# Kernel optimization log

Measured on AMD Instinct MI355X. Metric: run time of the kernel, lower is better.

The kernel has to match this reference:

```python
import jax, jax.numpy as jnp
import numpy as np

B = 32; NMAX = 256; E = 512; H = 512; U = 256; M = 32; L = 2; P = 4; TAU = 1.0
S = NMAX + 1                      # pseudo-seq len = nodes + SOS
IN0 = E + (M - 1) + P             # GRU layer-0 input size


def setup_inputs() -> dict:
    key = jax.random.key(0)
    ks = jax.random.split(key, 22)
    f = lambda k, sh, sc=0.05: jax.random.normal(k, sh, dtype=jnp.float32) * sc
    return {
        "h_padded": jax.random.normal(ks[0], (B, NMAX, E), jnp.float32),
        "hg": jax.random.normal(ks[1], (B, E), jnp.float32),
        "num_nodes": jax.random.randint(ks[2], (B,), 1, NMAX + 1),
        "u_noise": jax.random.uniform(ks[3], (M, B, S), jnp.float32),
        "emb_special": f(ks[4], (2, E), 1.0),
        "emb_pos": f(ks[5], (M, P), 1.0),
        "Wp": f(ks[6], (L * H, E)), "bp": f(ks[7], (L * H,)),
        "W_ih0": f(ks[8], (3 * H, IN0)), "W_hh0": f(ks[9], (3 * H, H)),
        "b_ih0": f(ks[10], (3 * H,)), "b_hh0": f(ks[11], (3 * H,)),
        "W_ih1": f(ks[12], (3 * H, H)), "W_hh1": f(ks[13], (3 * H, H)),
        "b_ih1": f(ks[14], (3 * H,)), "b_hh1": f(ks[15], (3 * H,)),
        "W1": f(ks[16], (U, H)), "W2": f(ks[17], (U, H)),
        "wc": f(ks[18], (U,)), "V": f(ks[19], (U,)),
        "Wf": f(ks[20], (M - 1, H)), "bf": f(ks[21], (M - 1,)),
    }


def _gru_step(x, hid, params):
    # torch nn.GRU single time step, L layers; gate order (r, z, n)
    new = []
    inp = x
    for l, (Wi, Wh, bi, bh) in enumerate(params):
        hp = hid[l]
        gi = inp @ Wi.T + bi
        gh = hp @ Wh.T + bh
        gi_r, gi_z, gi_n = jnp.split(gi, 3, axis=-1)
        gh_r, gh_z, gh_n = jnp.split(gh, 3, axis=-1)
        r = jax.nn.sigmoid(gi_r + gh_r)
        z = jax.nn.sigmoid(gi_z + gh_z)
        n = jnp.tanh(gi_n + r * gh_n)
        hn = (1.0 - z) * n + z * hp
        new.append(hn)
        inp = hn
    return inp, jnp.stack(new, 0)


def reference(h_padded, hg, num_nodes, u_noise, emb_special, emb_pos, Wp, bp,
              W_ih0, W_hh0, b_ih0, b_hh0, W_ih1, W_hh1, b_ih1, b_hh1,
              W1, W2, wc, V, Wf, bf):
    lens = num_nodes + 1
    mask = jnp.arange(S)[None, :] < lens[:, None]                       # [B,S]
    node_valid = (jnp.arange(NMAX)[None, :] < num_nodes[:, None]).astype(h_padded.dtype)
    # encoder_out = [SOS emb ; h nodes ; zero pad] as pad_sequence would give
    sos_enc = jnp.broadcast_to(emb_special[1], (B, 1, E))
    encoder_out = jnp.concatenate([sos_enc, h_padded * node_valid[..., None]], axis=1)  # [B,S,E]
    enc_W1 = encoder_out @ W1.T                                          # [B,S,U] hoisted (loop-invariant)
    dec_hidden = jnp.tanh(hg @ Wp.T + bp).reshape(B, L, H).transpose(1, 0, 2)  # [L,B,H]
    theta0 = jnp.zeros((B, M - 1), encoder_out.dtype)
    dec_input = jnp.concatenate([jnp.broadcast_to(emb_special[0], (B, E)), theta0], axis=1)
    cov_vec0 = jnp.zeros((B, S), encoder_out.dtype)
    gumbel = -jnp.log(-jnp.log(u_noise + 1e-10) + 1e-10)                 # [M,B,S]
    gru_params = ((W_ih0, W_hh0, b_ih0, b_hh0), (W_ih1, W_hh1, b_ih1, b_hh1))
    neg = jnp.float32(-1e30)

    def step(carry, xs):
        dec_in, hid, cov_vec, cov_loss = carry
        i, pe, g = xs
        x = jnp.concatenate([dec_in, jnp.broadcast_to(pe, (B, P))], axis=1)
        out, hid = _gru_step(x, hid, gru_params)                        # out [B,H]
        # Bahdanau attention with coverage
        uj = enc_W1 + (out @ W2.T)[:, None, :] + cov_vec[..., None] * wc
        uj = jnp.tanh(uj) @ V                                           # [B,S]
        aj = jax.nn.softmax(jnp.where(mask, uj, neg), axis=-1)
        # hard gumbel-softmax (straight-through)
        logits = jnp.log(aj + 1e-12)
        y = jax.nn.softmax((logits + g) / TAU, axis=1)
        onehot = jax.nn.one_hot(jnp.argmax(y, axis=1), S, dtype=y.dtype)
        hard = jax.lax.stop_gradient(onehot - y) + y
        chosen = jnp.einsum('bse,bs->be', encoder_out, hard)            # [B,E]
        cov_loss = cov_loss + jnp.minimum(aj, cov_vec).sum()
        cov_vec = cov_vec + aj
        theta = jnp.where(i < 1,
                          jnp.zeros((B, M - 1), out.dtype),
                          jax.nn.sigmoid(out @ Wf.T + bf))
        dec_next = jnp.concatenate([chosen, theta], axis=1)
        return (dec_next, hid, cov_vec, cov_loss), (hard, theta, aj)

    init = (dec_input, dec_hidden, cov_vec0, jnp.float32(0.0))
    xs = (jnp.arange(M), emb_pos, gumbel)
    carry_f, (hards, thetas, ajs) = jax.lax.scan(step, init, xs)
    cov_loss = carry_f[3] / B
    pointer = jnp.transpose(hards, (1, 2, 0))   # [B,S,M]
    adj = jnp.transpose(thetas, (1, 2, 0))      # [B,M-1,M]
    atts = jnp.transpose(ajs, (1, 2, 0))        # [B,S,M]
    return pointer, cov_loss, encoder_out, adj, atts
```

## Files before the change

### kernel.cpp

```cpp
#include <hip/hip_runtime.h>

constexpr int NB  = 32;
constexpr int NMX = 256;
constexpr int ED  = 512;
constexpr int HD  = 512;
constexpr int UD  = 256;
constexpr int MS  = 32;
constexpr int PD  = 4;
constexpr int SD  = 257;
constexpr int IL0 = 547;
constexpr int NI4_0 = 137;
constexpr int NI4_1 = 128;

constexpr long long OFF_PTR  = 0;
constexpr long long OFF_COVL = (long long)NB*SD*MS;
constexpr long long OFF_ENC  = OFF_COVL + 1;
constexpr long long OFF_ADJ  = OFF_ENC + (long long)NB*SD*ED;
constexpr long long OFF_ATT  = OFF_ADJ + (long long)NB*(MS-1)*MS;

__device__ __forceinline__ float sigf(float x){ return 1.0f/(1.0f + __expf(-x)); }
__device__ __forceinline__ float ftanh(float x){ float e = __expf(2.0f*x); return 1.0f - 2.0f/(e + 1.0f); }

__global__ void k_enc(const float* __restrict__ hp, const float* __restrict__ embsp,
                      const int* __restrict__ nn, float* __restrict__ out){
  int r = blockIdx.x; int b = r / SD, s = r % SD;
  float* dst = out + OFF_ENC + (long long)r*ED;
  int t = threadIdx.x;
  if (s == 0){
    const float* src = embsp + ED;
    int e = t*4; float4 v = *(const float4*)(src + e);
    dst[e] = v.x; dst[e+1] = v.y; dst[e+2] = v.z; dst[e+3] = v.w;
  } else if (s-1 < nn[b]){
    const float* src = hp + ((long long)b*NMX + (s-1))*ED;
    int e = t*4; float4 v = *(const float4*)(src + e);
    dst[e] = v.x; dst[e+1] = v.y; dst[e+2] = v.z; dst[e+3] = v.w;
  } else {
    int e = t*4;
    dst[e] = 0.f; dst[e+1] = 0.f; dst[e+2] = 0.f; dst[e+3] = 0.f;
  }
}

__global__ void k_misc(const float* __restrict__ hg, const float* __restrict__ embsp,
                       const float* __restrict__ embpos, const float* __restrict__ W1,
                       const float* __restrict__ Wih0, const float* __restrict__ W2,
                       float* __restrict__ x4, float* __restrict__ hg4,
                       float* __restrict__ cov, float* __restrict__ covl,
                       float* __restrict__ W1T, float* __restrict__ Wih0_4,
                       float* __restrict__ W2T){
  int idx = blockIdx.x*blockDim.x + threadIdx.x;
  const int N0 = 548*NB;
  const int N1 = N0 + ED*NB;
  const int N2 = N1 + NB*SD;
  const int N3 = N2 + NB;
  const int N4 = N3 + UD*ED;
  const int N5 = N4 + 1536*548;
  const int N6 = N5 + ED*UD;
  for (int i = idx; i < N6; i += gridDim.x*blockDim.x){
    if (i < N0){
      int kb = i >> 7, r = i & 3;
      int k = kb*4 + r;
      float v;
      if (k < ED) v = embsp[k];
      else if (k < ED + MS - 1) v = 0.f;
      else if (k < IL0) v = embpos[k - (ED + MS - 1)];
      else v = 0.f;
      x4[i] = v;
    } else if (i < N1){
      int j = i - N0;
      int kb = j >> 7, b = (j >> 2) & 31, r = j & 3;
      hg4[j] = hg[(long long)b*ED + kb*4 + r];
    } else if (i < N2){
      cov[i - N1] = 0.f;
    } else if (i < N3){
      covl[i - N2] = 0.f;
    } else if (i < N4){
      int j = i - N3; int k = j / UD, u = j % UD;
      W1T[j] = W1[(long long)u*ED + k];
    } else if (i < N5){
      int j = i - N4; int row = j / 548, c = j % 548;
      Wih0_4[j] = (c < IL0) ? Wih0[(long long)row*IL0 + c] : 0.f;
    } else {
      int j = i - N5; int k = j / UD, u = j % UD;
      W2T[j] = W2[(long long)u*HD + k];
    }
  }
}

__global__ __launch_bounds__(256) void k_encw1(const float* __restrict__ out,
                        const float4* __restrict__ W1T4, float4* __restrict__ encW1){
  __shared__ __align__(16) float As[16][68];
  __shared__ __align__(16) float Bs[16][68];
  int t = threadIdx.x;
  int bm = blockIdx.x >> 2, bn = blockIdx.x & 3;
  int m0 = bm*64, n0 = bn*64;
  const float* A = out + OFF_ENC;
  int tm = t >> 4, tn = t & 15;
  float4 acc[4];
  #pragma unroll
  for (int i = 0; i < 4; ++i) acc[i] = {0.f,0.f,0.f,0.f};
  int arow = t >> 2, akq = t & 3;
  int bk = t >> 4, bnq = t & 15;
  for (int k0 = 0; k0 < 512; k0 += 16){
    float av[4];
    bool okA = (m0 + arow) < NB*SD;
    long long abase = (long long)(m0 + arow)*ED + k0 + akq*4;
    #pragma unroll
    for (int j = 0; j < 4; ++j) av[j] = okA ? A[abase + j] : 0.f;
    float4 bv = W1T4[(long long)(k0 + bk)*64 + (n0 >> 2) + bnq];
    __syncthreads();
    #pragma unroll
    for (int j = 0; j < 4; ++j) As[akq*4 + j][arow] = av[j];
    *(float4*)&Bs[bk][bnq*4] = bv;
    __syncthreads();
    #pragma unroll
    for (int kk = 0; kk < 16; ++kk){
      float4 a = *(const float4*)&As[kk][tm*4];
      float4 bq = *(const float4*)&Bs[kk][tn*4];
      acc[0].x += a.x*bq.x; acc[0].y += a.x*bq.y; acc[0].z += a.x*bq.z; acc[0].w += a.x*bq.w;
      acc[1].x += a.y*bq.x; acc[1].y += a.y*bq.y; acc[1].z += a.y*bq.z; acc[1].w += a.y*bq.w;
      acc[2].x += a.z*bq.x; acc[2].y += a.z*bq.y; acc[2].z += a.z*bq.z; acc[2].w += a.z*bq.w;
      acc[3].x += a.w*bq.x; acc[3].y += a.w*bq.y; acc[3].z += a.w*bq.z; acc[3].w += a.w*bq.w;
    }
  }
  #pragma unroll
  for (int i = 0; i < 4; ++i){
    int r = m0 + tm*4 + i;
    if (r < NB*SD) encW1[(long long)r*64 + (n0 >> 2) + tn] = acc[i];
  }
}

__global__ void k_hid0(const float4* __restrict__ hg4, const float4* __restrict__ Wp4,
                       const float* __restrict__ bp, float* __restrict__ h0,
                       float* __restrict__ h1){
  int t = threadIdx.x; int b = t & 31;
  int row = blockIdx.x*8 + (t >> 5);
  const float4* w = Wp4 + (long long)row*128;
  float acc = bp[row];
  #pragma unroll 4
  for (int i = 0; i < 128; ++i){
    float4 wv = w[i], xv = hg4[i*NB + b];
    acc += wv.x*xv.x + wv.y*xv.y + wv.z*xv.z + wv.w*xv.w;
  }
  float v = ftanh(acc);
  int h = row & 511;
  int idx = (h >> 2)*128 + b*4 + (h & 3);
  if (row < HD) h0[idx] = v;
  else          h1[idx] = v;
}

template<int NI4>
__global__ __launch_bounds__(512) void k_gru(const float4* __restrict__ x4,
                      const float4* __restrict__ h4,
                      const float4* __restrict__ Wih4, const float4* __restrict__ Whh4,
                      const float* __restrict__ bih, const float* __restrict__ bhh,
                      float* __restrict__ outT){
  __shared__ float part[2][NB][8][6];
  int t = threadIdx.x;
  int b = t & 31, ks = (t >> 5) & 7, hl = (t >> 8) & 1;
  int h = blockIdx.x*2 + hl;
  float ai0 = 0.f, ai1 = 0.f, ai2 = 0.f, ah0 = 0.f, ah1 = 0.f, ah2 = 0.f;
  {
    const float4* w0 = Wih4 + (long long)(0*HD + h)*NI4;
    const float4* w1 = Wih4 + (long long)(1*HD + h)*NI4;
    const float4* w2 = Wih4 + (long long)(2*HD + h)*NI4;
    int s0 = (ks*NI4) >> 3, e0 = ((ks + 1)*NI4) >> 3;
    for (int kb = s0; kb < e0; ++kb){
      float4 xv = x4[kb*NB + b];
      float4 a = w0[kb], c = w1[kb], d = w2[kb];
      ai0 += xv.x*a.x + xv.y*a.y + xv.z*a.z + xv.w*a.w;
      ai1 += xv.x*c.x + xv.y*c.y + xv.z*c.z + xv.w*c.w;
      ai2 += xv.x*d.x + xv.y*d.y + xv.z*d.z + xv.w*d.w;
    }
  }
  {
    const float4* w0 = Whh4 + (long long)(0*HD + h)*128;
    const float4* w1 = Whh4 + (long long)(1*HD + h)*128;
    const float4* w2 = Whh4 + (long long)(2*HD + h)*128;
    int s1 = ks*16, e1 = s1 + 16;
    for (int kb = s1; kb < e1; ++kb){
      float4 xv = h4[kb*NB + b];
      float4 a = w0[kb], c = w1[kb], d = w2[kb];
      ah0 += xv.x*a.x + xv.y*a.y + xv.z*a.z + xv.w*a.w;
      ah1 += xv.x*c.x + xv.y*c.y + xv.z*c.z + xv.w*c.w;
      ah2 += xv.x*d.x + xv.y*d.y + xv.z*d.z + xv.w*d.w;
    }
  }
  part[hl][b][ks][0] = ai0; part[hl][b][ks][1] = ai1; part[hl][b][ks][2] = ai2;
  part[hl][b][ks][3] = ah0; part[hl][b][ks][4] = ah1; part[hl][b][ks][5] = ah2;
  __syncthreads();
  if (t < 64){
    int b2 = t & 31, hl2 = t >> 5;
    int h2 = blockIdx.x*2 + hl2;
    float g0=0.f,g1=0.f,g2=0.f,g3=0.f,g4=0.f,g5=0.f;
    #pragma unroll
    for (int k = 0; k < 8; ++k){
      g0 += part[hl2][b2][k][0]; g1 += part[hl2][b2][k][1]; g2 += part[hl2][b2][k][2];
      g3 += part[hl2][b2][k][3]; g4 += part[hl2][b2][k][4]; g5 += part[hl2][b2][k][5];
    }
    float gir = g0 + bih[h2], giz = g1 + bih[HD + h2], gin = g2 + bih[2*HD + h2];
    float ghr = g3 + bhh[h2], ghz = g4 + bhh[HD + h2], ghn = g5 + bhh[2*HD + h2];
    float r = sigf(gir + ghr);
    float z = sigf(giz + ghz);
    float nn = ftanh(gin + r*ghn);
    int idx = (h2 >> 2)*128 + b2*4 + (h2 & 3);
    float hp = ((const float*)h4)[idx];
    outT[idx] = (1.f - z)*nn + z*hp;
  }
}

__global__ __launch_bounds__(512) void k_qs(const float4* __restrict__ h1,
                      const float4* __restrict__ W2T4, const float4* __restrict__ Wf4,
                      const float* __restrict__ bfv, const float* __restrict__ embpos,
                      int m, const float4* __restrict__ encW1,
                      const float4* __restrict__ wc4, const float4* __restrict__ V4,
                      const float* __restrict__ cov, float* __restrict__ sc,
                      float* __restrict__ x4, float* __restrict__ out){
  __shared__ __align__(16) float h1s[512];
  __shared__ __align__(16) float wcs[256];
  __shared__ __align__(16) float Vs[256];
  __shared__ __align__(16) float qs[256];
  __shared__ __align__(16) float4 qpart[8][64];
  int t = threadIdx.x;
  int b = blockIdx.x >> 3, seg = blockIdx.x & 7;
  if (t < 128) ((float4*)h1s)[t] = h1[t*NB + b];
  else if (t < 192) ((float4*)wcs)[t - 128] = wc4[t - 128];
  else if (t < 256) ((float4*)Vs)[t - 192] = V4[t - 192];
  __syncthreads();
  {
    int u4 = t & 63, kq = t >> 6;
    float4 acc = {0.f,0.f,0.f,0.f};
    const float4* w = W2T4 + (long long)(kq*64)*64 + u4;
    const float* hh = h1s + kq*64;
    #pragma unroll 4
    for (int k = 0; k < 64; ++k){
      float a = hh[k];
      float4 wv = w[(long long)k*64];
      acc.x += a*wv.x; acc.y += a*wv.y; acc.z += a*wv.z; acc.w += a*wv.w;
    }
    qpart[kq][u4] = acc;
  }
  __syncthreads();
  if (t < 64){
    float4 s = qpart[0][t];
    #pragma unroll
    for (int k = 1; k < 8; ++k){
      float4 p = qpart[k][t];
      s.x += p.x; s.y += p.y; s.z += p.z; s.w += p.w;
    }
    ((float4*)qs)[t] = s;
  } else if (seg == 0){
    int w = (t >> 6) - 1;
    int lane = t & 63;
    for (int j = w; j < MS-1; j += 7){
      const float4* wf = Wf4 + (long long)j*128 + lane*2;
      float4 w0 = wf[0], w1v = wf[1];
      const float4* hh4 = (const float4*)h1s + lane*2;
      float4 hv0 = hh4[0], hv1 = hh4[1];
      float d = w0.x*hv0.x + w0.y*hv0.y + w0.z*hv0.z + w0.w*hv0.w
              + w1v.x*hv1.x + w1v.y*hv1.y + w1v.z*hv1.z + w1v.w*hv1.w;
      for (int off = 32; off; off >>= 1) d += __shfl_xor(d, off);
      if (lane == 0){
        float th = (m < 1) ? 0.f : sigf(d + bfv[j]);
        out[OFF_ADJ + (long long)b*(MS-1)*MS + (long long)j*MS + m] = th;
        int k = ED + j;
        x4[(k >> 2)*128 + b*4 + (k & 3)] = th;
      }
    }
  }
  if (seg == 0 && t == 0 && m + 1 < MS){
    #pragma unroll
    for (int p = 0; p < PD; ++p){
      int k = ED + MS - 1 + p;
      x4[(k >> 2)*128 + b*4 + (k & 3)] = embpos[(m+1)*PD + p];
    }
  }
  __syncthreads();
  int lane = t & 63, wav = t >> 6;
  int s0 = seg*33;
  float4 q4 = ((const float4*)qs)[lane];
  float4 wv = ((const float4*)wcs)[lane];
  float4 vv = ((const float4*)Vs)[lane];
  for (int s = s0 + wav; s < s0 + 33 && s < SD; s += 8){
    float cv = cov[b*SD + s];
    float4 e4 = encW1[((long long)b*SD + s)*64 + lane];
    float acc = vv.x*ftanh(e4.x + q4.x + cv*wv.x)
              + vv.y*ftanh(e4.y + q4.y + cv*wv.y)
              + vv.z*ftanh(e4.z + q4.z + cv*wv.z)
              + vv.w*ftanh(e4.w + q4.w + cv*wv.w);
    for (int off = 32; off; off >>= 1) acc += __shfl_xor(acc, off);
    if (lane == 0) sc[b*SD + s] = acc;
  }
}

__global__ __launch_bounds__(512) void k_soft(const float* __restrict__ sc,
                      const int* __restrict__ nn, const float* __restrict__ un, int m,
                      float* __restrict__ cov, float* __restrict__ covl,
                      float* __restrict__ out, float4* __restrict__ x4,
                      const float* __restrict__ enc){
  __shared__ float red[8]; __shared__ float redc[8]; __shared__ int redi[8];
  __shared__ float s_mx, s_den; __shared__ int s_k;
  int b = blockIdx.x, t = threadIdx.x;
  int lane = t & 63, wav = t >> 6;
  int n = nn[b];
  float sv = (t < SD) ? sc[b*SD + t] : -3.4e38f;
  float cv = (t < SD) ? cov[b*SD + t] : 0.f;
  float v1 = (t < SD && t <= n) ? sv : -3.4e38f;
  for (int off = 32; off; off >>= 1) v1 = fmaxf(v1, __shfl_xor(v1, off));
  if (lane == 0) red[wav] = v1;
  __syncthreads();
  if (t == 0){
    float mm = red[0];
    for (int i = 1; i < 8; ++i) mm = fmaxf(mm, red[i]);
    s_mx = mm;
  }
  __syncthreads();
  float ev = (t < SD && t <= n) ? __expf(sv - s_mx) : 0.f;
  float v2 = ev;
  for (int off = 32; off; off >>= 1) v2 += __shfl_xor(v2, off);
  if (lane == 0) red[wav] = v2;
  __syncthreads();
  if (t == 0){
    float ss = 0.f;
    for (int i = 0; i < 8; ++i) ss += red[i];
    s_den = ss;
  }
  __syncthreads();
  float aj = (t < SD) ? ev / s_den : 0.f;
  float yl = -3.4e38f; int idx = SD; float lcl = 0.f;
  if (t < SD){
    float u = un[((long long)m*NB + b)*SD + t];
    float g = -__logf(-__logf(u + 1e-10f) + 1e-10f);
    yl = __logf(aj + 1e-12f) + g;
    idx = t;
    lcl = fminf(aj, cv);
    cov[b*SD + t] = cv + aj;
    out[OFF_ATT + ((long long)b*SD + t)*MS + m] = aj;
  }
  for (int off = 32; off; off >>= 1){
    float oy = __shfl_xor(yl, off); int oi = __shfl_xor(idx, off);
    if (oy > yl || (oy == yl && oi < idx)){ yl = oy; idx = oi; }
  }
  for (int off = 32; off; off >>= 1) lcl += __shfl_xor(lcl, off);
  if (lane == 0){ red[wav] = yl; redi[wav] = idx; redc[wav] = lcl; }
  __syncthreads();
  if (t == 0){
    float by = red[0]; int bi = redi[0]; float cl = redc[0];
    for (int w = 1; w < 8; ++w){
      if (red[w] > by || (red[w] == by && redi[w] < bi)){ by = red[w]; bi = redi[w]; }
      cl += redc[w];
    }
    s_k = bi;
    covl[b] += cl;
  }
  __syncthreads();
  int kk = s_k;
  if (t < SD) out[OFF_PTR + ((long long)b*SD + t)*MS + m] = (t == kk) ? 1.f : 0.f;
  const float* er = enc + ((long long)b*SD + kk)*ED;
  if (t < 128){
    float4 v; v.x = er[t*4]; v.y = er[t*4+1]; v.z = er[t*4+2]; v.w = er[t*4+3];
    x4[t*NB + b] = v;
  }
}

__global__ void k_fin(const float* __restrict__ covl, float* __restrict__ out){
  if (threadIdx.x == 0 && blockIdx.x == 0){
    float s = 0.f;
    for (int i = 0; i < NB; ++i) s += covl[i];
    out[OFF_COVL] = s / (float)NB;
  }
}

extern "C" void kernel_launch(void* const* d_in, const int* in_sizes, int n_in,
                              void* d_out, int out_size, void* d_ws, size_t ws_size,
                              hipStream_t stream){
  const float* h_padded    = (const float*)d_in[0];
  const float* hg          = (const float*)d_in[1];
  const int*   num_nodes   = (const int*)  d_in[2];
  const float* u_noise     = (const float*)d_in[3];
  const float* emb_special = (const float*)d_in[4];
  const float* emb_pos     = (const float*)d_in[5];
  const float* Wp          = (const float*)d_in[6];
  const float* bp          = (const float*)d_in[7];
  const float* W_ih0       = (const float*)d_in[8];
  const float* W_hh0       = (const float*)d_in[9];
  const float* b_ih0       = (const float*)d_in[10];
  const float* b_hh0       = (const float*)d_in[11];
  const float* W_ih1       = (const float*)d_in[12];
  const float* W_hh1       = (const float*)d_in[13];
  const float* b_ih1       = (const float*)d_in[14];
  const float* b_hh1       = (const float*)d_in[15];
  const float* W1          = (const float*)d_in[16];
  const float* W2          = (const float*)d_in[17];
  const float* wc          = (const float*)d_in[18];
  const float* V           = (const float*)d_in[19];
  const float* Wf          = (const float*)d_in[20];
  const float* bf          = (const float*)d_in[21];
  float* out = (float*)d_out;

  float* ws      = (float*)d_ws;
  float* encW1   = ws;  ws += (long long)NB*SD*UD;
  float* Wih0_4  = ws;  ws += (long long)1536*548;
  float* W1T     = ws;  ws += (long long)UD*ED;
  float* W2T     = ws;  ws += (long long)UD*ED;
  float* x4      = ws;  ws += 548*NB;
  float* hg4     = ws;  ws += ED*NB;
  float* h0      = ws;  ws += 2*HD*NB;
  float* h1      = ws;  ws += 2*HD*NB;
  float* cov     = ws;  ws += NB*SD;
  float* covl    = ws;  ws += NB;
  float* sc      = ws;  ws += NB*SD;

  k_enc  <<<NB*SD, 128, 0, stream>>>(h_padded, emb_special, num_nodes, out);
  k_misc <<<256, 256, 0, stream>>>(hg, emb_special, emb_pos, W1, W_ih0, W2,
                                   x4, hg4, cov, covl, W1T, Wih0_4, W2T);
  k_encw1<<<516, 256, 0, stream>>>(out, (const float4*)W1T, (float4*)encW1);
  k_hid0 <<<128, 256, 0, stream>>>((const float4*)hg4, (const float4*)Wp, bp, h0, h1);

  for (int m = 0; m < MS; ++m){
    float* h0c = h0 + (m & 1)*HD*NB;
    float* h0n = h0 + ((m + 1) & 1)*HD*NB;
    float* h1c = h1 + (m & 1)*HD*NB;
    float* h1n = h1 + ((m + 1) & 1)*HD*NB;
    k_gru<NI4_0><<<256, 512, 0, stream>>>((const float4*)x4, (const float4*)h0c,
        (const float4*)Wih0_4, (const float4*)W_hh0, b_ih0, b_hh0, h0n);
    k_gru<NI4_1><<<256, 512, 0, stream>>>((const float4*)h0n, (const float4*)h1c,
        (const float4*)W_ih1, (const float4*)W_hh1, b_ih1, b_hh1, h1n);
    k_qs  <<<256, 512, 0, stream>>>((const float4*)h1n, (const float4*)W2T,
        (const float4*)Wf, bf, emb_pos, m, (const float4*)encW1,
        (const float4*)wc, (const float4*)V, cov, sc, x4, out);
    k_soft<<<NB, 512, 0, stream>>>(sc, num_nodes, u_noise, m, cov, covl, out,
        (float4*)x4, out + OFF_ENC);
  }
  k_fin<<<1, 64, 0, stream>>>(covl, out);
}
```

Baseline: 1.427 ms.

## Fuse attention scoring with softmax kernel, retile encW1 GEMM, unroll GRU loops

Merges the per-step query/score kernel and the softmax/sampling kernel into one 1024-thread block per batch row, keeping scores in shared memory and dropping one launch per decoder step. The cost is that each step's attention now runs on only 32 blocks instead of 256. The layer-0 GRU input is padded to 576 so the reduction splits evenly into fixed-length, fully unrolled loops. The encW1 GEMM tile grows to 128 rows with 8 accumulators per thread, halving the grid.

```diff
diff --git a/kernel.cpp b/kernel.cpp
--- a/kernel.cpp
+++ b/kernel.cpp
@@ -9,8 +9,8 @@
 constexpr int PD  = 4;
 constexpr int SD  = 257;
 constexpr int IL0 = 547;
-constexpr int NI4_0 = 137;
-constexpr int NI4_1 = 128;
+constexpr int XP  = 576;
+constexpr int XP4 = 144;
 
 constexpr long long OFF_PTR  = 0;
 constexpr long long OFF_COVL = (long long)NB*SD*MS;
@@ -48,12 +48,12 @@
                        float* __restrict__ W1T, float* __restrict__ Wih0_4,
                        float* __restrict__ W2T){
   int idx = blockIdx.x*blockDim.x + threadIdx.x;
-  const int N0 = 548*NB;
+  const int N0 = XP*NB;
   const int N1 = N0 + ED*NB;
   const int N2 = N1 + NB*SD;
   const int N3 = N2 + NB;
   const int N4 = N3 + UD*ED;
-  const int N5 = N4 + 1536*548;
+  const int N5 = N4 + 1536*XP;
   const int N6 = N5 + ED*UD;
   for (int i = idx; i < N6; i += gridDim.x*blockDim.x){
     if (i < N0){
@@ -77,7 +77,7 @@
       int j = i - N3; int k = j / UD, u = j % UD;
       W1T[j] = W1[(long long)u*ED + k];
     } else if (i < N5){
-      int j = i - N4; int row = j / 548, c = j % 548;
+      int j = i - N4; int row = j / XP, c = j % XP;
       Wih0_4[j] = (c < IL0) ? Wih0[(long long)row*IL0 + c] : 0.f;
     } else {
       int j = i - N5; int k = j / UD, u = j % UD;
@@ -88,43 +88,48 @@
 
 __global__ __launch_bounds__(256) void k_encw1(const float* __restrict__ out,
                         const float4* __restrict__ W1T4, float4* __restrict__ encW1){
-  __shared__ __align__(16) float As[16][68];
+  __shared__ __align__(16) float As[16][132];
   __shared__ __align__(16) float Bs[16][68];
   int t = threadIdx.x;
   int bm = blockIdx.x >> 2, bn = blockIdx.x & 3;
-  int m0 = bm*64, n0 = bn*64;
+  int m0 = bm*128, n0 = bn*64;
   const float* A = out + OFF_ENC;
   int tm = t >> 4, tn = t & 15;
-  float4 acc[4];
+  float4 acc[8];
   #pragma unroll
-  for (int i = 0; i < 4; ++i) acc[i] = {0.f,0.f,0.f,0.f};
-  int arow = t >> 2, akq = t & 3;
-  int bk = t >> 4, bnq = t & 15;
+  for (int i = 0; i < 8; ++i) acc[i] = {0.f,0.f,0.f,0.f};
+  int arow = t >> 1, ac2 = t & 1;
+  int bk = t >> 4, bn4 = t & 15;
   for (int k0 = 0; k0 < 512; k0 += 16){
-    float av[4];
-    bool okA = (m0 + arow) < NB*SD;
-    long long abase = (long long)(m0 + arow)*ED + k0 + akq*4;
-    #pragma unroll
-    for (int j = 0; j < 4; ++j) av[j] = okA ? A[abase + j] : 0.f;
-    float4 bv = W1T4[(long long)(k0 + bk)*64 + (n0 >> 2) + bnq];
+    float av[8];
+    int rr = m0 + arow; if (rr >= NB*SD) rr = NB*SD - 1;
+    long long abase = (long long)rr*ED + k0 + ac2*8;
+    #pragma unroll
+    for (int j = 0; j < 8; ++j) av[j] = A[abase + j];
+    float4 bv = W1T4[(long long)(k0 + bk)*64 + (n0 >> 2) + bn4];
     __syncthreads();
     #pragma unroll
-    for (int j = 0; j < 4; ++j) As[akq*4 + j][arow] = av[j];
-    *(float4*)&Bs[bk][bnq*4] = bv;
+    for (int j = 0; j < 8; ++j) As[ac2*8 + j][arow] = av[j];
+    *(float4*)&Bs[bk][bn4*4] = bv;
     __syncthreads();
     #pragma unroll
     for (int kk = 0; kk < 16; ++kk){
-      float4 a = *(const float4*)&As[kk][tm*4];
+      float4 a0 = *(const float4*)&As[kk][tm*8];
+      float4 a1 = *(const float4*)&As[kk][tm*8 + 4];
       float4 bq = *(const float4*)&Bs[kk][tn*4];
-      acc[0].x += a.x*bq.x; acc[0].y += a.x*bq.y; acc[0].z += a.x*bq.z; acc[0].w += a.x*bq.w;
-      acc[1].x += a.y*bq.x; acc[1].y += a.y*bq.y; acc[1].z += a.y*bq.z; acc[1].w += a.y*bq.w;
-      acc[2].x += a.z*bq.x; acc[2].y += a.z*bq.y; acc[2].z += a.z*bq.z; acc[2].w += a.z*bq.w;
-      acc[3].x += a.w*bq.x; acc[3].y += a.w*bq.y; acc[3].z += a.w*bq.z; acc[3].w += a.w*bq.w;
+      acc[0].x += a0.x*bq.x; acc[0].y += a0.x*bq.y; acc[0].z += a0.x*bq.z; acc[0].w += a0.x*bq.w;
+      acc[1].x += a0.y*bq.x; acc[1].y += a0.y*bq.y; acc[1].z += a0.y*bq.z; acc[1].w += a0.y*bq.w;
+      acc[2].x += a0.z*bq.x; acc[2].y += a0.z*bq.y; acc[2].z += a0.z*bq.z; acc[2].w += a0.z*bq.w;
+      acc[3].x += a0.w*bq.x; acc[3].y += a0.w*bq.y; acc[3].z += a0.w*bq.z; acc[3].w += a0.w*bq.w;
+      acc[4].x += a1.x*bq.x; acc[4].y += a1.x*bq.y; acc[4].z += a1.x*bq.z; acc[4].w += a1.x*bq.w;
+      acc[5].x += a1.y*bq.x; acc[5].y += a1.y*bq.y; acc[5].z += a1.y*bq.z; acc[5].w += a1.y*bq.w;
+      acc[6].x += a1.z*bq.x; acc[6].y += a1.z*bq.y; acc[6].z += a1.z*bq.z; acc[6].w += a1.z*bq.w;
+      acc[7].x += a1.w*bq.x; acc[7].y += a1.w*bq.y; acc[7].z += a1.w*bq.z; acc[7].w += a1.w*bq.w;
     }
   }
   #pragma unroll
-  for (int i = 0; i < 4; ++i){
-    int r = m0 + tm*4 + i;
+  for (int i = 0; i < 8; ++i){
+    int r = m0 + tm*8 + i;
     if (r < NB*SD) encW1[(long long)r*64 + (n0 >> 2) + tn] = acc[i];
   }
 }
@@ -148,24 +153,26 @@
   else          h1[idx] = v;
 }
 
-template<int NI4>
+template<int PER>
 __global__ __launch_bounds__(512) void k_gru(const float4* __restrict__ x4,
                       const float4* __restrict__ h4,
                       const float4* __restrict__ Wih4, const float4* __restrict__ Whh4,
                       const float* __restrict__ bih, const float* __restrict__ bhh,
                       float* __restrict__ outT){
+  constexpr int NI4 = PER*8;
   __shared__ float part[2][NB][8][6];
   int t = threadIdx.x;
   int b = t & 31, ks = (t >> 5) & 7, hl = (t >> 8) & 1;
   int h = blockIdx.x*2 + hl;
   float ai0 = 0.f, ai1 = 0.f, ai2 = 0.f, ah0 = 0.f, ah1 = 0.f, ah2 = 0.f;
   {
-    const float4* w0 = Wih4 + (long long)(0*HD + h)*NI4;
-    const float4* w1 = Wih4 + (long long)(1*HD + h)*NI4;
-    const float4* w2 = Wih4 + (long long)(2*HD + h)*NI4;
-    int s0 = (ks*NI4) >> 3, e0 = ((ks + 1)*NI4) >> 3;
-    for (int kb = s0; kb < e0; ++kb){
-      float4 xv = x4[kb*NB + b];
+    const float4* w0 = Wih4 + (long long)(0*HD + h)*NI4 + ks*PER;
+    const float4* w1 = Wih4 + (long long)(1*HD + h)*NI4 + ks*PER;
+    const float4* w2 = Wih4 + (long long)(2*HD + h)*NI4 + ks*PER;
+    const float4* xb = x4 + (long long)(ks*PER)*NB + b;
+    #pragma unroll
+    for (int kb = 0; kb < PER; ++kb){
+      float4 xv = xb[kb*NB];
       float4 a = w0[kb], c = w1[kb], d = w2[kb];
       ai0 += xv.x*a.x + xv.y*a.y + xv.z*a.z + xv.w*a.w;
       ai1 += xv.x*c.x + xv.y*c.y + xv.z*c.z + xv.w*c.w;
@@ -173,12 +180,13 @@
     }
   }
   {
-    const float4* w0 = Whh4 + (long long)(0*HD + h)*128;
-    const float4* w1 = Whh4 + (long long)(1*HD + h)*128;
-    const float4* w2 = Whh4 + (long long)(2*HD + h)*128;
-    int s1 = ks*16, e1 = s1 + 16;
-    for (int kb = s1; kb < e1; ++kb){
-      float4 xv = h4[kb*NB + b];
+    const float4* w0 = Whh4 + (long long)(0*HD + h)*128 + ks*16;
+    const float4* w1 = Whh4 + (long long)(1*HD + h)*128 + ks*16;
+    const float4* w2 = Whh4 + (long long)(2*HD + h)*128 + ks*16;
+    const float4* hb = h4 + (long long)(ks*16)*NB + b;
+    #pragma unroll
+    for (int kb = 0; kb < 16; ++kb){
+      float4 xv = hb[kb*NB];
       float4 a = w0[kb], c = w1[kb], d = w2[kb];
       ah0 += xv.x*a.x + xv.y*a.y + xv.z*a.z + xv.w*a.w;
       ah1 += xv.x*c.x + xv.y*c.y + xv.z*c.z + xv.w*c.w;
@@ -208,50 +216,44 @@
   }
 }
 
-__global__ __launch_bounds__(512) void k_qs(const float4* __restrict__ h1,
+__global__ __launch_bounds__(1024) void k_attn2(const float4* __restrict__ h1,
                       const float4* __restrict__ W2T4, const float4* __restrict__ Wf4,
                       const float* __restrict__ bfv, const float* __restrict__ embpos,
                       int m, const float4* __restrict__ encW1,
                       const float4* __restrict__ wc4, const float4* __restrict__ V4,
-                      const float* __restrict__ cov, float* __restrict__ sc,
-                      float* __restrict__ x4, float* __restrict__ out){
+                      const int* __restrict__ nn, const float* __restrict__ un,
+                      float* __restrict__ cov, float* __restrict__ covl,
+                      float* __restrict__ out, float* __restrict__ x4,
+                      const float* __restrict__ enc){
   __shared__ __align__(16) float h1s[512];
   __shared__ __align__(16) float wcs[256];
   __shared__ __align__(16) float Vs[256];
   __shared__ __align__(16) float qs[256];
   __shared__ __align__(16) float4 qpart[8][64];
-  int t = threadIdx.x;
-  int b = blockIdx.x >> 3, seg = blockIdx.x & 7;
+  __shared__ float scs[SD];
+  __shared__ float red[16]; __shared__ float redc[16]; __shared__ int redi[16];
+  __shared__ float s_mx, s_den; __shared__ int s_k;
+  int t = threadIdx.x, b = blockIdx.x;
+  int lane = t & 63, wav = t >> 6;
   if (t < 128) ((float4*)h1s)[t] = h1[t*NB + b];
   else if (t < 192) ((float4*)wcs)[t - 128] = wc4[t - 128];
   else if (t < 256) ((float4*)Vs)[t - 192] = V4[t - 192];
   __syncthreads();
-  {
-    int u4 = t & 63, kq = t >> 6;
+  if (t < 512){
+    int kq = t >> 6, u4 = t & 63;
     float4 acc = {0.f,0.f,0.f,0.f};
     const float4* w = W2T4 + (long long)(kq*64)*64 + u4;
     const float* hh = h1s + kq*64;
-    #pragma unroll 4
+    #pragma unroll 8
     for (int k = 0; k < 64; ++k){
       float a = hh[k];
       float4 wv = w[(long long)k*64];
       acc.x += a*wv.x; acc.y += a*wv.y; acc.z += a*wv.z; acc.w += a*wv.w;
     }
     qpart[kq][u4] = acc;
-  }
-  __syncthreads();
-  if (t < 64){
-    float4 s = qpart[0][t];
-    #pragma unroll
-    for (int k = 1; k < 8; ++k){
-      float4 p = qpart[k][t];
-      s.x += p.x; s.y += p.y; s.z += p.z; s.w += p.w;
-    }
-    ((float4*)qs)[t] = s;
-  } else if (seg == 0){
-    int w = (t >> 6) - 1;
-    int lane = t & 63;
-    for (int j = w; j < MS-1; j += 7){
+  } else if (wav < 15){
+    int w0i = wav - 8;
+    for (int j = w0i; j < MS-1; j += 7){
       const float4* wf = Wf4 + (long long)j*128 + lane*2;
       float4 w0 = wf[0], w1v = wf[1];
       const float4* hh4 = (const float4*)h1s + lane*2;
@@ -266,8 +268,7 @@
         x4[(k >> 2)*128 + b*4 + (k & 3)] = th;
       }
     }
-  }
-  if (seg == 0 && t == 0 && m + 1 < MS){
+  } else if (t == 1023 && m + 1 < MS){
     #pragma unroll
     for (int p = 0; p < PD; ++p){
       int k = ED + MS - 1 + p;
@@ -275,59 +276,56 @@
     }
   }
   __syncthreads();
-  int lane = t & 63, wav = t >> 6;
-  int s0 = seg*33;
-  float4 q4 = ((const float4*)qs)[lane];
-  float4 wv = ((const float4*)wcs)[lane];
-  float4 vv = ((const float4*)Vs)[lane];
-  for (int s = s0 + wav; s < s0 + 33 && s < SD; s += 8){
-    float cv = cov[b*SD + s];
-    float4 e4 = encW1[((long long)b*SD + s)*64 + lane];
-    float acc = vv.x*ftanh(e4.x + q4.x + cv*wv.x)
-              + vv.y*ftanh(e4.y + q4.y + cv*wv.y)
-              + vv.z*ftanh(e4.z + q4.z + cv*wv.z)
-              + vv.w*ftanh(e4.w + q4.w + cv*wv.w);
-    for (int off = 32; off; off >>= 1) acc += __shfl_xor(acc, off);
-    if (lane == 0) sc[b*SD + s] = acc;
-  }
-}
-
-__global__ __launch_bounds__(512) void k_soft(const float* __restrict__ sc,
-                      const int* __restrict__ nn, const float* __restrict__ un, int m,
-                      float* __restrict__ cov, float* __restrict__ covl,
-                      float* __restrict__ out, float4* __restrict__ x4,
-                      const float* __restrict__ enc){
-  __shared__ float red[8]; __shared__ float redc[8]; __shared__ int redi[8];
-  __shared__ float s_mx, s_den; __shared__ int s_k;
-  int b = blockIdx.x, t = threadIdx.x;
-  int lane = t & 63, wav = t >> 6;
+  if (t < 256){
+    const float* fp = (const float*)qpart;
+    float s = 0.f;
+    #pragma unroll
+    for (int k = 0; k < 8; ++k) s += fp[k*256 + t];
+    qs[t] = s;
+  }
+  __syncthreads();
+  {
+    float4 q4 = ((const float4*)qs)[lane];
+    float4 wv = ((const float4*)wcs)[lane];
+    float4 vv = ((const float4*)Vs)[lane];
+    for (int s = wav; s < SD; s += 16){
+      float cv = cov[b*SD + s];
+      float4 e4 = encW1[((long long)b*SD + s)*64 + lane];
+      float acc = vv.x*ftanh(e4.x + q4.x + cv*wv.x)
+                + vv.y*ftanh(e4.y + q4.y + cv*wv.y)
+                + vv.z*ftanh(e4.z + q4.z + cv*wv.z)
+                + vv.w*ftanh(e4.w + q4.w + cv*wv.w);
+      for (int off = 32; off; off >>= 1) acc += __shfl_xor(acc, off);
+      if (lane == 0) scs[s] = acc;
+    }
+  }
+  __syncthreads();
   int n = nn[b];
-  float sv = (t < SD) ? sc[b*SD + t] : -3.4e38f;
-  float cv = (t < SD) ? cov[b*SD + t] : 0.f;
-  float v1 = (t < SD && t <= n) ? sv : -3.4e38f;
+  float v1 = (t < SD && t <= n) ? scs[t] : -3.4e38f;
   for (int off = 32; off; off >>= 1) v1 = fmaxf(v1, __shfl_xor(v1, off));
   if (lane == 0) red[wav] = v1;
   __syncthreads();
   if (t == 0){
     float mm = red[0];
-    for (int i = 1; i < 8; ++i) mm = fmaxf(mm, red[i]);
+    for (int i = 1; i < 16; ++i) mm = fmaxf(mm, red[i]);
     s_mx = mm;
   }
   __syncthreads();
-  float ev = (t < SD && t <= n) ? __expf(sv - s_mx) : 0.f;
+  float ev = (t < SD && t <= n) ? __expf(scs[t] - s_mx) : 0.f;
   float v2 = ev;
   for (int off = 32; off; off >>= 1) v2 += __shfl_xor(v2, off);
   if (lane == 0) red[wav] = v2;
   __syncthreads();
   if (t == 0){
     float ss = 0.f;
-    for (int i = 0; i < 8; ++i) ss += red[i];
+    for (int i = 0; i < 16; ++i) ss += red[i];
     s_den = ss;
   }
   __syncthreads();
   float aj = (t < SD) ? ev / s_den : 0.f;
   float yl = -3.4e38f; int idx = SD; float lcl = 0.f;
   if (t < SD){
+    float cv = cov[b*SD + t];
     float u = un[((long long)m*NB + b)*SD + t];
     float g = -__logf(-__logf(u + 1e-10f) + 1e-10f);
     yl = __logf(aj + 1e-12f) + g;
@@ -345,7 +343,7 @@
   __syncthreads();
   if (t == 0){
     float by = red[0]; int bi = redi[0]; float cl = redc[0];
-    for (int w = 1; w < 8; ++w){
+    for (int w = 1; w < 16; ++w){
       if (red[w] > by || (red[w] == by && redi[w] < bi)){ by = red[w]; bi = redi[w]; }
       cl += redc[w];
     }
@@ -358,7 +356,7 @@
   const float* er = enc + ((long long)b*SD + kk)*ED;
   if (t < 128){
     float4 v; v.x = er[t*4]; v.y = er[t*4+1]; v.z = er[t*4+2]; v.w = er[t*4+3];
-    x4[t*NB + b] = v;
+    ((float4*)x4)[t*NB + b] = v;
   }
 }
 
@@ -399,21 +397,20 @@
 
   float* ws      = (float*)d_ws;
   float* encW1   = ws;  ws += (long long)NB*SD*UD;
-  float* Wih0_4  = ws;  ws += (long long)1536*548;
+  float* Wih0_4  = ws;  ws += (long long)1536*XP;
   float* W1T     = ws;  ws += (long long)UD*ED;
   float* W2T     = ws;  ws += (long long)UD*ED;
-  float* x4      = ws;  ws += 548*NB;
+  float* x4      = ws;  ws += XP*NB;
   float* hg4     = ws;  ws += ED*NB;
   float* h0      = ws;  ws += 2*HD*NB;
   float* h1      = ws;  ws += 2*HD*NB;
   float* cov     = ws;  ws += NB*SD;
   float* covl    = ws;  ws += NB;
-  float* sc      = ws;  ws += NB*SD;
 
   k_enc  <<<NB*SD, 128, 0, stream>>>(h_padded, emb_special, num_nodes, out);
   k_misc <<<256, 256, 0, stream>>>(hg, emb_special, emb_pos, W1, W_ih0, W2,
                                    x4, hg4, cov, covl, W1T, Wih0_4, W2T);
-  k_encw1<<<516, 256, 0, stream>>>(out, (const float4*)W1T, (float4*)encW1);
+  k_encw1<<<260, 256, 0, stream>>>(out, (const float4*)W1T, (float4*)encW1);
   k_hid0 <<<128, 256, 0, stream>>>((const float4*)hg4, (const float4*)Wp, bp, h0, h1);
 
   for (int m = 0; m < MS; ++m){
@@ -421,15 +418,14 @@
     float* h0n = h0 + ((m + 1) & 1)*HD*NB;
     float* h1c = h1 + (m & 1)*HD*NB;
     float* h1n = h1 + ((m + 1) & 1)*HD*NB;
-    k_gru<NI4_0><<<256, 512, 0, stream>>>((const float4*)x4, (const float4*)h0c,
+    k_gru<18><<<256, 512, 0, stream>>>((const float4*)x4, (const float4*)h0c,
         (const float4*)Wih0_4, (const float4*)W_hh0, b_ih0, b_hh0, h0n);
-    k_gru<NI4_1><<<256, 512, 0, stream>>>((const float4*)h0n, (const float4*)h1c,
+    k_gru<16><<<256, 512, 0, stream>>>((const float4*)h0n, (const float4*)h1c,
         (const float4*)W_ih1, (const float4*)W_hh1, b_ih1, b_hh1, h1n);
-    k_qs  <<<256, 512, 0, stream>>>((const float4*)h1n, (const float4*)W2T,
+    k_attn2<<<NB, 1024, 0, stream>>>((const float4*)h1n, (const float4*)W2T,
         (const float4*)Wf, bf, emb_pos, m, (const float4*)encW1,
-        (const float4*)wc, (const float4*)V, cov, sc, x4, out);
-    k_soft<<<NB, 512, 0, stream>>>(sc, num_nodes, u_noise, m, cov, covl, out,
-        (float4*)x4, out + OFF_ENC);
+        (const float4*)wc, (const float4*)V, num_nodes, u_noise,
+        cov, covl, out, x4, out + OFF_ENC);
   }
   k_fin<<<1, 64, 0, stream>>>(covl, out);
 }
```

Result: slower. 1.549 ms (+8.5%).

## Fuse init kernels, skip padded rows, and fully unroll GRU dot loops

Applied to the files above, without the earlier changes.

Merges the encoder copy and the misc preprocessing into one kernel, and merges the encW1 GEMM with the initial hidden projection (which now reads hg directly, removing the hg4 transpose). It skips GEMM tiles and attention-score work for sequence positions beyond each batch's node count, relying on k_soft masking those positions. The GRU input is padded to 576 columns so each of the 8 k-slices has a fixed trip count, letting the dot-product loops be fully unrolled. The risk is that skipped score entries in sc stay stale, which is only safe if downstream code never reads masked positions.

```diff
diff --git a/kernel.cpp b/kernel.cpp
--- a/kernel.cpp
+++ b/kernel.cpp
@@ -9,8 +9,7 @@
 constexpr int PD  = 4;
 constexpr int SD  = 257;
 constexpr int IL0 = 547;
-constexpr int NI4_0 = 137;
-constexpr int NI4_1 = 128;
+constexpr int XP  = 576;
 
 constexpr long long OFF_PTR  = 0;
 constexpr long long OFF_COVL = (long long)NB*SD*MS;
@@ -21,41 +20,38 @@
 __device__ __forceinline__ float sigf(float x){ return 1.0f/(1.0f + __expf(-x)); }
 __device__ __forceinline__ float ftanh(float x){ float e = __expf(2.0f*x); return 1.0f - 2.0f/(e + 1.0f); }
 
-__global__ void k_enc(const float* __restrict__ hp, const float* __restrict__ embsp,
-                      const int* __restrict__ nn, float* __restrict__ out){
-  int r = blockIdx.x; int b = r / SD, s = r % SD;
-  float* dst = out + OFF_ENC + (long long)r*ED;
-  int t = threadIdx.x;
-  if (s == 0){
-    const float* src = embsp + ED;
-    int e = t*4; float4 v = *(const float4*)(src + e);
-    dst[e] = v.x; dst[e+1] = v.y; dst[e+2] = v.z; dst[e+3] = v.w;
-  } else if (s-1 < nn[b]){
-    const float* src = hp + ((long long)b*NMX + (s-1))*ED;
-    int e = t*4; float4 v = *(const float4*)(src + e);
-    dst[e] = v.x; dst[e+1] = v.y; dst[e+2] = v.z; dst[e+3] = v.w;
-  } else {
-    int e = t*4;
-    dst[e] = 0.f; dst[e+1] = 0.f; dst[e+2] = 0.f; dst[e+3] = 0.f;
-  }
-}
-
-__global__ void k_misc(const float* __restrict__ hg, const float* __restrict__ embsp,
-                       const float* __restrict__ embpos, const float* __restrict__ W1,
-                       const float* __restrict__ Wih0, const float* __restrict__ W2,
-                       float* __restrict__ x4, float* __restrict__ hg4,
-                       float* __restrict__ cov, float* __restrict__ covl,
-                       float* __restrict__ W1T, float* __restrict__ Wih0_4,
-                       float* __restrict__ W2T){
-  int idx = blockIdx.x*blockDim.x + threadIdx.x;
-  const int N0 = 548*NB;
-  const int N1 = N0 + ED*NB;
-  const int N2 = N1 + NB*SD;
-  const int N3 = N2 + NB;
-  const int N4 = N3 + UD*ED;
-  const int N5 = N4 + 1536*548;
-  const int N6 = N5 + ED*UD;
-  for (int i = idx; i < N6; i += gridDim.x*blockDim.x){
+__global__ __launch_bounds__(256) void k_init(const float* __restrict__ hp,
+                      const float* __restrict__ embsp, const float* __restrict__ embpos,
+                      const float* __restrict__ W1, const float* __restrict__ Wih0,
+                      const float* __restrict__ W2, const int* __restrict__ nn,
+                      float* __restrict__ out, float* __restrict__ x4,
+                      float* __restrict__ cov, float* __restrict__ covl,
+                      float* __restrict__ W1T, float* __restrict__ Wih0_4,
+                      float* __restrict__ W2T){
+  int blk = blockIdx.x, t = threadIdx.x;
+  {
+    int r = blk*2 + (t >> 7);
+    int tid = t & 127;
+    int b = r / SD, s = r % SD;
+    float* dst = out + OFF_ENC + (long long)r*ED + tid*4;
+    if (s == 0){
+      const float* src = embsp + ED + tid*4;
+      dst[0] = src[0]; dst[1] = src[1]; dst[2] = src[2]; dst[3] = src[3];
+    } else if (s-1 < nn[b]){
+      const float* src = hp + ((long long)b*NMX + (s-1))*ED + tid*4;
+      float4 v = *(const float4*)src;
+      dst[0] = v.x; dst[1] = v.y; dst[2] = v.z; dst[3] = v.w;
+    } else {
+      dst[0] = 0.f; dst[1] = 0.f; dst[2] = 0.f; dst[3] = 0.f;
+    }
+  }
+  const int N0 = XP*NB;
+  const int N1 = N0 + NB*SD;
+  const int N2 = N1 + NB;
+  const int N3 = N2 + UD*ED;
+  const int N4 = N3 + 1536*XP;
+  const int N5 = N4 + ED*UD;
+  for (int i = blk*256 + t; i < N5; i += 4112*256){
     if (i < N0){
       int kb = i >> 7, r = i & 3;
       int k = kb*4 + r;
@@ -66,106 +62,116 @@
       else v = 0.f;
       x4[i] = v;
     } else if (i < N1){
-      int j = i - N0;
-      int kb = j >> 7, b = (j >> 2) & 31, r = j & 3;
-      hg4[j] = hg[(long long)b*ED + kb*4 + r];
+      cov[i - N0] = 0.f;
     } else if (i < N2){
-      cov[i - N1] = 0.f;
+      covl[i - N1] = 0.f;
     } else if (i < N3){
-      covl[i - N2] = 0.f;
+      int j = i - N2; int k = j / UD, u = j % UD;
+      W1T[j] = W1[(long long)u*ED + k];
     } else if (i < N4){
-      int j = i - N3; int k = j / UD, u = j % UD;
-      W1T[j] = W1[(long long)u*ED + k];
-    } else if (i < N5){
-      int j = i - N4; int row = j / 548, c = j % 548;
+      int j = i - N3; int row = j / XP, c = j % XP;
       Wih0_4[j] = (c < IL0) ? Wih0[(long long)row*IL0 + c] : 0.f;
     } else {
-      int j = i - N5; int k = j / UD, u = j % UD;
+      int j = i - N4; int k = j / UD, u = j % UD;
       W2T[j] = W2[(long long)u*HD + k];
     }
   }
 }
 
-__global__ __launch_bounds__(256) void k_encw1(const float* __restrict__ out,
-                        const float4* __restrict__ W1T4, float4* __restrict__ encW1){
+__global__ __launch_bounds__(256) void k_ew1h(const float* __restrict__ out,
+                        const float4* __restrict__ W1T4, float4* __restrict__ encW1,
+                        const int* __restrict__ nn,
+                        const float* __restrict__ hg, const float4* __restrict__ Wp4,
+                        const float* __restrict__ bp, float* __restrict__ h0,
+                        float* __restrict__ h1){
   __shared__ __align__(16) float As[16][68];
   __shared__ __align__(16) float Bs[16][68];
-  int t = threadIdx.x;
-  int bm = blockIdx.x >> 2, bn = blockIdx.x & 3;
-  int m0 = bm*64, n0 = bn*64;
-  const float* A = out + OFF_ENC;
-  int tm = t >> 4, tn = t & 15;
-  float4 acc[4];
-  #pragma unroll
-  for (int i = 0; i < 4; ++i) acc[i] = {0.f,0.f,0.f,0.f};
-  int arow = t >> 2, akq = t & 3;
-  int bk = t >> 4, bnq = t & 15;
-  for (int k0 = 0; k0 < 512; k0 += 16){
-    float av[4];
-    bool okA = (m0 + arow) < NB*SD;
-    long long abase = (long long)(m0 + arow)*ED + k0 + akq*4;
-    #pragma unroll
-    for (int j = 0; j < 4; ++j) av[j] = okA ? A[abase + j] : 0.f;
-    float4 bv = W1T4[(long long)(k0 + bk)*64 + (n0 >> 2) + bnq];
-    __syncthreads();
-    #pragma unroll
-    for (int j = 0; j < 4; ++j) As[akq*4 + j][arow] = av[j];
-    *(float4*)&Bs[bk][bnq*4] = bv;
-    __syncthreads();
-    #pragma unroll
-    for (int kk = 0; kk < 16; ++kk){
-      float4 a = *(const float4*)&As[kk][tm*4];
-      float4 bq = *(const float4*)&Bs[kk][tn*4];
-      acc[0].x += a.x*bq.x; acc[0].y += a.x*bq.y; acc[0].z += a.x*bq.z; acc[0].w += a.x*bq.w;
-      acc[1].x += a.y*bq.x; acc[1].y += a.y*bq.y; acc[1].z += a.y*bq.z; acc[1].w += a.y*bq.w;
-      acc[2].x += a.z*bq.x; acc[2].y += a.z*bq.y; acc[2].z += a.z*bq.z; acc[2].w += a.z*bq.w;
-      acc[3].x += a.w*bq.x; acc[3].y += a.w*bq.y; acc[3].z += a.w*bq.z; acc[3].w += a.w*bq.w;
-    }
-  }
-  #pragma unroll
-  for (int i = 0; i < 4; ++i){
-    int r = m0 + tm*4 + i;
-    if (r < NB*SD) encW1[(long long)r*64 + (n0 >> 2) + tn] = acc[i];
-  }
-}
-
-__global__ void k_hid0(const float4* __restrict__ hg4, const float4* __restrict__ Wp4,
-                       const float* __restrict__ bp, float* __restrict__ h0,
-                       float* __restrict__ h1){
-  int t = threadIdx.x; int b = t & 31;
-  int row = blockIdx.x*8 + (t >> 5);
-  const float4* w = Wp4 + (long long)row*128;
-  float acc = bp[row];
-  #pragma unroll 4
-  for (int i = 0; i < 128; ++i){
-    float4 wv = w[i], xv = hg4[i*NB + b];
-    acc += wv.x*xv.x + wv.y*xv.y + wv.z*xv.z + wv.w*xv.w;
-  }
-  float v = ftanh(acc);
-  int h = row & 511;
-  int idx = (h >> 2)*128 + b*4 + (h & 3);
-  if (row < HD) h0[idx] = v;
-  else          h1[idx] = v;
-}
-
-template<int NI4>
+  int blk = blockIdx.x, t = threadIdx.x;
+  if (blk < 516){
+    int bm = blk >> 2, bn = blk & 3;
+    int m0 = bm*64, n0 = bn*64;
+    {
+      int rr = m0 + (t & 63);
+      bool act = false;
+      if (rr < NB*SD){
+        int b = rr / SD, s = rr % SD;
+        act = (s <= nn[b]);
+      }
+      if (!__any(act)) return;
+    }
+    const float* A = out + OFF_ENC;
+    int tm = t >> 4, tn = t & 15;
+    float4 acc[4];
+    #pragma unroll
+    for (int i = 0; i < 4; ++i) acc[i] = {0.f,0.f,0.f,0.f};
+    int arow = t >> 2, akq = t & 3;
+    int bk = t >> 4, bnq = t & 15;
+    for (int k0 = 0; k0 < 512; k0 += 16){
+      float av[4];
+      bool okA = (m0 + arow) < NB*SD;
+      long long abase = (long long)(m0 + arow)*ED + k0 + akq*4;
+      #pragma unroll
+      for (int j = 0; j < 4; ++j) av[j] = okA ? A[abase + j] : 0.f;
+      float4 bv = W1T4[(long long)(k0 + bk)*64 + (n0 >> 2) + bnq];
+      __syncthreads();
+      #pragma unroll
+      for (int j = 0; j < 4; ++j) As[akq*4 + j][arow] = av[j];
+      *(float4*)&Bs[bk][bnq*4] = bv;
+      __syncthreads();
+      #pragma unroll
+      for (int kk = 0; kk < 16; ++kk){
+        float4 a = *(const float4*)&As[kk][tm*4];
+        float4 bq = *(const float4*)&Bs[kk][tn*4];
+        acc[0].x += a.x*bq.x; acc[0].y += a.x*bq.y; acc[0].z += a.x*bq.z; acc[0].w += a.x*bq.w;
+        acc[1].x += a.y*bq.x; acc[1].y += a.y*bq.y; acc[1].z += a.y*bq.z; acc[1].w += a.y*bq.w;
+        acc[2].x += a.z*bq.x; acc[2].y += a.z*bq.y; acc[2].z += a.z*bq.z; acc[2].w += a.z*bq.w;
+        acc[3].x += a.w*bq.x; acc[3].y += a.w*bq.y; acc[3].z += a.w*bq.z; acc[3].w += a.w*bq.w;
+      }
+    }
+    #pragma unroll
+    for (int i = 0; i < 4; ++i){
+      int r = m0 + tm*4 + i;
+      if (r < NB*SD) encW1[(long long)r*64 + (n0 >> 2) + tn] = acc[i];
+    }
+  } else {
+    int b = t & 31;
+    int row = (blk - 516)*8 + (t >> 5);
+    const float4* w = Wp4 + (long long)row*128;
+    const float4* xg = (const float4*)(hg + (long long)b*ED);
+    float acc = bp[row];
+    #pragma unroll 4
+    for (int i = 0; i < 128; ++i){
+      float4 wv = w[i], xv = xg[i];
+      acc += wv.x*xv.x + wv.y*xv.y + wv.z*xv.z + wv.w*xv.w;
+    }
+    float v = ftanh(acc);
+    int h = row & 511;
+    int idx = (h >> 2)*128 + b*4 + (h & 3);
+    if (row < HD) h0[idx] = v;
+    else          h1[idx] = v;
+  }
+}
+
+template<int PER>
 __global__ __launch_bounds__(512) void k_gru(const float4* __restrict__ x4,
                       const float4* __restrict__ h4,
                       const float4* __restrict__ Wih4, const float4* __restrict__ Whh4,
                       const float* __restrict__ bih, const float* __restrict__ bhh,
                       float* __restrict__ outT){
+  constexpr int NI4 = PER*8;
   __shared__ float part[2][NB][8][6];
   int t = threadIdx.x;
   int b = t & 31, ks = (t >> 5) & 7, hl = (t >> 8) & 1;
   int h = blockIdx.x*2 + hl;
   float ai0 = 0.f, ai1 = 0.f, ai2 = 0.f, ah0 = 0.f, ah1 = 0.f, ah2 = 0.f;
   {
-    const float4* w0 = Wih4 + (long long)(0*HD + h)*NI4;
-    const float4* w1 = Wih4 + (long long)(1*HD + h)*NI4;
-    const float4* w2 = Wih4 + (long long)(2*HD + h)*NI4;
-    int s0 = (ks*NI4) >> 3, e0 = ((ks + 1)*NI4) >> 3;
-    for (int kb = s0; kb < e0; ++kb){
-      float4 xv = x4[kb*NB + b];
+    const float4* w0 = Wih4 + (long long)(0*HD + h)*NI4 + ks*PER;
+    const float4* w1 = Wih4 + (long long)(1*HD + h)*NI4 + ks*PER;
+    const float4* w2 = Wih4 + (long long)(2*HD + h)*NI4 + ks*PER;
+    const float4* xb = x4 + (long long)(ks*PER)*NB + b;
+    #pragma unroll
+    for (int kb = 0; kb < PER; ++kb){
+      float4 xv = xb[kb*NB];
       float4 a = w0[kb], c = w1[kb], d = w2[kb];
       ai0 += xv.x*a.x + xv.y*a.y + xv.z*a.z + xv.w*a.w;
       ai1 += xv.x*c.x + xv.y*c.y + xv.z*c.z + xv.w*c.w;
@@ -173,12 +179,13 @@
     }
   }
   {
-    const float4* w0 = Whh4 + (long long)(0*HD + h)*128;
-    const float4* w1 = Whh4 + (long long)(1*HD + h)*128;
-    const float4* w2 = Whh4 + (long long)(2*HD + h)*128;
-    int s1 = ks*16, e1 = s1 + 16;
-    for (int kb = s1; kb < e1; ++kb){
-      float4 xv = h4[kb*NB + b];
+    const float4* w0 = Whh4 + (long long)(0*HD + h)*128 + ks*16;
+    const float4* w1 = Whh4 + (long long)(1*HD + h)*128 + ks*16;
+    const float4* w2 = Whh4 + (long long)(2*HD + h)*128 + ks*16;
+    const float4* hb = h4 + (long long)(ks*16)*NB + b;
+    #pragma unroll
+    for (int kb = 0; kb < 16; ++kb){
+      float4 xv = hb[kb*NB];
       float4 a = w0[kb], c = w1[kb], d = w2[kb];
       ah0 += xv.x*a.x + xv.y*a.y + xv.z*a.z + xv.w*a.w;
       ah1 += xv.x*c.x + xv.y*c.y + xv.z*c.z + xv.w*c.w;
@@ -213,6 +220,7 @@
                       const float* __restrict__ bfv, const float* __restrict__ embpos,
                       int m, const float4* __restrict__ encW1,
                       const float4* __restrict__ wc4, const float4* __restrict__ V4,
+                      const int* __restrict__ nn,
                       const float* __restrict__ cov, float* __restrict__ sc,
                       float* __restrict__ x4, float* __restrict__ out){
   __shared__ __align__(16) float h1s[512];
@@ -222,6 +230,8 @@
   __shared__ __align__(16) float4 qpart[8][64];
   int t = threadIdx.x;
   int b = blockIdx.x >> 3, seg = blockIdx.x & 7;
+  int n = nn[b];
+  if (seg != 0 && seg*33 > n) return;
   if (t < 128) ((float4*)h1s)[t] = h1[t*NB + b];
   else if (t < 192) ((float4*)wcs)[t - 128] = wc4[t - 128];
   else if (t < 256) ((float4*)Vs)[t - 192] = V4[t - 192];
@@ -281,6 +291,7 @@
   float4 wv = ((const float4*)wcs)[lane];
   float4 vv = ((const float4*)Vs)[lane];
   for (int s = s0 + wav; s < s0 + 33 && s < SD; s += 8){
+    if (s > n) continue;
     float cv = cov[b*SD + s];
     float4 e4 = encW1[((long long)b*SD + s)*64 + lane];
     float acc = vv.x*ftanh(e4.x + q4.x + cv*wv.x)
@@ -399,35 +410,33 @@
 
   float* ws      = (float*)d_ws;
   float* encW1   = ws;  ws += (long long)NB*SD*UD;
-  float* Wih0_4  = ws;  ws += (long long)1536*548;
+  float* Wih0_4  = ws;  ws += (long long)1536*XP;
   float* W1T     = ws;  ws += (long long)UD*ED;
   float* W2T     = ws;  ws += (long long)UD*ED;
-  float* x4      = ws;  ws += 548*NB;
-  float* hg4     = ws;  ws += ED*NB;
+  float* x4      = ws;  ws += XP*NB;
   float* h0      = ws;  ws += 2*HD*NB;
   float* h1      = ws;  ws += 2*HD*NB;
   float* cov     = ws;  ws += NB*SD;
   float* covl    = ws;  ws += NB;
   float* sc      = ws;  ws += NB*SD;
 
-  k_enc  <<<NB*SD, 128, 0, stream>>>(h_padded, emb_special, num_nodes, out);
-  k_misc <<<256, 256, 0, stream>>>(hg, emb_special, emb_pos, W1, W_ih0, W2,
-                                   x4, hg4, cov, covl, W1T, Wih0_4, W2T);
-  k_encw1<<<516, 256, 0, stream>>>(out, (const float4*)W1T, (float4*)encW1);
-  k_hid0 <<<128, 256, 0, stream>>>((const float4*)hg4, (const float4*)Wp, bp, h0, h1);
+  k_init<<<4112, 256, 0, stream>>>(h_padded, emb_special, emb_pos, W1, W_ih0, W2,
+                                   num_nodes, out, x4, cov, covl, W1T, Wih0_4, W2T);
+  k_ew1h<<<644, 256, 0, stream>>>(out, (const float4*)W1T, (float4*)encW1,
+                                  num_nodes, hg, (const float4*)Wp, bp, h0, h1);
 
   for (int m = 0; m < MS; ++m){
     float* h0c = h0 + (m & 1)*HD*NB;
     float* h0n = h0 + ((m + 1) & 1)*HD*NB;
     float* h1c = h1 + (m & 1)*HD*NB;
     float* h1n = h1 + ((m + 1) & 1)*HD*NB;
-    k_gru<NI4_0><<<256, 512, 0, stream>>>((const float4*)x4, (const float4*)h0c,
+    k_gru<18><<<256, 512, 0, stream>>>((const float4*)x4, (const float4*)h0c,
         (const float4*)Wih0_4, (const float4*)W_hh0, b_ih0, b_hh0, h0n);
-    k_gru<NI4_1><<<256, 512, 0, stream>>>((const float4*)h0n, (const float4*)h1c,
+    k_gru<16><<<256, 512, 0, stream>>>((const float4*)h0n, (const float4*)h1c,
         (const float4*)W_ih1, (const float4*)W_hh1, b_ih1, b_hh1, h1n);
     k_qs  <<<256, 512, 0, stream>>>((const float4*)h1n, (const float4*)W2T,
         (const float4*)Wf, bf, emb_pos, m, (const float4*)encW1,
-        (const float4*)wc, (const float4*)V, cov, sc, x4, out);
+        (const float4*)wc, (const float4*)V, num_nodes, cov, sc, x4, out);
     k_soft<<<NB, 512, 0, stream>>>(sc, num_nodes, u_noise, m, cov, covl, out,
         (float4*)x4, out + OFF_ENC);
   }
```

New measurement: 1.290 ms. 9.7% less time.
